# Optimization experiments

Hardware: AMD Instinct MI355X
Metric: run time of the kernel (lower is better)

Reference implementation:

```python
import jax, jax.numpy as jnp
import numpy as np

C, V, L, P, E, HM, H, M, B, T = 512, 32000, 2, 2, 8, 1024, 8, 256, 2, 1024
TOPK, RATIO = 2, 0.5


def setup_inputs() -> dict:
    key = jax.random.key(0)
    ks = iter(jax.random.split(key, 64))

    def nrm(shape, s=0.02):
        return (jax.random.normal(next(ks), shape) * s).astype(jnp.float32)

    return {
        "ids": jax.random.randint(next(ks), (B, T), 0, V, dtype=jnp.int32),
        "embed_w": nrm((V, C)),
        "mem": nrm((M, C)),
        "mp_w": nrm((2 * C, C)), "mp_b": jnp.zeros((C,), jnp.float32),
        "qkv_w": nrm((L, P, C, 3 * C)), "qkv_b": jnp.zeros((L, P, 3 * C), jnp.float32),
        "aw_w": nrm((L, P, C, H)), "aw_b": jnp.zeros((L, P, H), jnp.float32),
        "dscale": jnp.ones((L, P), jnp.float32),
        "mg_w": nrm((L, P * C, C)), "mg_b": jnp.zeros((L, C), jnp.float32),
        "ln_g": jnp.ones((L, C), jnp.float32), "ln_b": jnp.zeros((L, C), jnp.float32),
        "gw": nrm((L, C, E)), "gb": jnp.zeros((L, E), jnp.float32),
        "ew1": nrm((L, E, C, HM)), "eb1": jnp.zeros((L, E, HM), jnp.float32),
        "ew2": nrm((L, E, HM, C)), "eb2": jnp.zeros((L, E, C), jnp.float32),
        "q1w": nrm((L, C, 4 * C)), "q1b": jnp.zeros((L, 4 * C), jnp.float32),
        "q2w": nrm((L, 4 * C, 1)), "q2b": jnp.zeros((L, 1), jnp.float32),
        "errw": nrm((L, C, C)), "errb": jnp.zeros((L, C), jnp.float32),
        "ag1w": nrm((2 * C, 4 * C)), "ag1b": jnp.zeros((4 * C,), jnp.float32),
        "ag2w": nrm((4 * C, C)), "ag2b": jnp.zeros((C,), jnp.float32),
        "pscale": jnp.ones((C,), jnp.float32),
        "head_w": nrm((C, V)), "head_b": jnp.zeros((V,), jnp.float32),
    }


def _forward(ids, embed_w, mem, mp_w, mp_b, qkv_w, qkv_b, aw_w, aw_b, dscale,
             mg_w, mg_b, ln_g, ln_b, gw, gb, ew1, eb1, ew2, eb2,
             q1w, q1b, q2w, q2b, errw, errb, ag1w, ag1b, ag2w, ag2b,
             pscale, head_w, head_b):
    b, t = ids.shape
    hd = C // H
    x = embed_w[ids]                                        # [B,T,C] embedding gather
    # DynamicMemoryBank: attention over memory slots, concat retrieved
    en = jnp.einsum('btc,mc->btm', x, mem)
    ret = jnp.einsum('btm,mc->btc', jax.nn.softmax(en, -1), mem)
    x = jnp.concatenate([x, ret], -1) @ mp_w + mp_b         # memory_proj
    for l in range(L):
        x_in = x
        # IterativeReasoningBlock: stacked MetaCognitiveAttention phases
        h = x_in
        prior = None
        outs = []
        for p in range(P):
            qkv = (h @ qkv_w[l, p] + qkv_b[l, p]).reshape(b, t, 3, H, hd)
            q, k, v = (jnp.moveaxis(qkv[:, :, i], 1, 2) for i in range(3))  # [B,H,T,hd]
            aware = (h.mean(1) @ aw_w[l, p] + aw_b[l, p])[:, :, None, None]  # [B,H,1,1]
            attn = jax.nn.softmax(
                jnp.einsum('bhtd,bhsd->bhts', q, k) * (dscale[l, p] * aware), -1)
            if prior is not None:
                attn = attn + 0.3 * prior
            prior = jax.lax.stop_gradient(attn)
            o = jnp.einsum('bhts,bhsd->bthd', attn, v).reshape(b, t, C)
            h = jax.nn.silu(o)
            outs.append(h)
        merged = jnp.concatenate(outs, -1) @ mg_w[l] + mg_b[l]
        z = merged + x_in
        mu = z.mean(-1, keepdims=True)
        xn = (z - mu) / jnp.sqrt(z.var(-1, keepdims=True) + 1e-5) * ln_g[l] + ln_b[l]
        # MoE: softmax gate, top-k routing, combine (dense-equivalent math)
        scores = jax.nn.softmax(xn @ gw[l] + gb[l], -1)     # [B,T,E]
        vals, idx = jax.lax.top_k(scores, TOPK)
        w = jnp.sum(jax.nn.one_hot(idx, E, dtype=xn.dtype) * vals[..., None], axis=-2)
        eh = jnp.einsum('btc,ech->bteh', xn, ew1[l]) + eb1[l]
        eh = eh * jax.nn.silu(eh)                           # swiglu act: x*silu(x)
        ey = jnp.einsum('bteh,ehc->btec', eh, ew2[l]) + eb2[l]
        moe_out = jnp.einsum('btec,bte->btc', ey, w)
        reason = xn + moe_out * RATIO
        # IntrospectionLayer (quality estimator sees detached x)
        quality = jax.nn.sigmoid(
            jax.nn.silu(jax.lax.stop_gradient(x_in) @ q1w[l] + q1b[l]) @ q2w[l] + q2b[l])
        intro = x_in + 0.3 * ((x_in * (1.0 - quality)) @ errw[l] + errb[l])
        # AutonomousLearningGate
        gate = jnp.tanh(
            jax.nn.silu(jnp.concatenate([reason, intro], -1) @ ag1w + ag1b) @ ag2w + ag2b)
        x = reason + gate * pscale * intro
    return x @ head_w + head_b                              # [B,T,V]


def reference(ids, embed_w, mem, mp_w, mp_b, qkv_w, qkv_b, aw_w, aw_b, dscale,
              mg_w, mg_b, ln_g, ln_b, gw, gb, ew1, eb1, ew2, eb2,
              q1w, q1b, q2w, q2b, errw, errb, ag1w, ag1b, ag2w, ag2b,
              pscale, head_w, head_b):
    return _forward(ids, embed_w, mem, mp_w, mp_b, qkv_w, qkv_b, aw_w, aw_b, dscale,
                    mg_w, mg_b, ln_g, ln_b, gw, gb, ew1, eb1, ew2, eb2,
                    q1w, q1b, q2w, q2b, errw, errb, ag1w, ag1b, ag2w, ag2b,
                    pscale, head_w, head_b)
```

## Files before the change

kernel.cpp:

```cpp
#include <hip/hip_runtime.h>


#define NTOK 2048
#define CDIM 512
#define TLEN 1024
#define NB 2
#define NH 8
#define VDIM 32000

typedef __attribute__((ext_vector_type(4))) float f32x4;
typedef __attribute__((ext_vector_type(8))) __bf16 bf16x8;
typedef __attribute__((ext_vector_type(4))) __bf16 bf16x4;

#define AS1 __attribute__((address_space(1)))
#define AS3 __attribute__((address_space(3)))

__device__ __forceinline__ void g2lds16(const void* g, void* l) {
    __builtin_amdgcn_global_load_lds((const AS1 void*)g, (AS3 void*)l, 16, 0, 0);
}

__global__ __launch_bounds__(256) void gemm_bf16(
    const __bf16* __restrict__ A, int lda,
    const __bf16* __restrict__ B,
    float* __restrict__ C_, int ldc,
    __bf16* __restrict__ Cb, int ldcb,
    const float* __restrict__ bias,
    const float* __restrict__ res, int ldres, float alpha,
    int K, int act)
{
    __shared__ __align__(16) char smem[16384];
    __bf16* As = (__bf16*)smem;
    __bf16* Bs = (__bf16*)(smem + 8192);
    float* cs = (float*)smem;
    const int tid = threadIdx.x;
    const int w = tid >> 6, lane = tid & 63;
    const int nwg = gridDim.x;
    const int q = nwg >> 3, r = nwg & 7;
    const int xcd = blockIdx.x & 7, ii = blockIdx.x >> 3;
    const int swz = (xcd < r) ? xcd * (q + 1) + ii : r * (q + 1) + (xcd - r) * q + ii;
    const int m0 = (swz & 15) * 128, n0 = (swz >> 4) * 128;
    const int wr = (w >> 1) * 64, wc = (w & 1) * 64;
    f32x4 acc[4][4] = {};
    const int mrow = lane & 15, kq = (lane >> 4) * 8;
    for (int k0 = 0; k0 < K; k0 += 32) {
#pragma unroll
        for (int i = 0; i < 2; ++i) {
            const int boff = w * 2048 + i * 1024 + lane * 16;
            const int row = boff >> 6;
            const int ke = (boff & 63) >> 1;
            g2lds16(A + (long)(m0 + row) * lda + k0 + ke, (char*)As + (boff - lane * 16));
            g2lds16(B + (long)(n0 + row) * K + k0 + ke, (char*)Bs + (boff - lane * 16));
        }
        __syncthreads();
        bf16x8 af[4], bfr[4];
#pragma unroll
        for (int i = 0; i < 4; ++i)
            af[i] = *(const bf16x8*)(As + (wr + i * 16 + mrow) * 32 + kq);
#pragma unroll
        for (int j = 0; j < 4; ++j)
            bfr[j] = *(const bf16x8*)(Bs + (wc + j * 16 + mrow) * 32 + kq);
#pragma unroll
        for (int i = 0; i < 4; ++i)
#pragma unroll
            for (int j = 0; j < 4; ++j)
                acc[i][j] = __builtin_amdgcn_mfma_f32_16x16x32_bf16(af[i], bfr[j], acc[i][j], 0, 0, 0);
        __syncthreads();
    }
    const int col_l = lane & 15, row_l = (lane >> 4) * 4;
#pragma unroll
    for (int p = 0; p < 4; ++p) {
        if ((w >> 1) == (p >> 1)) {
#pragma unroll
            for (int iq = 0; iq < 2; ++iq) {
                const int i = (p & 1) * 2 + iq;
#pragma unroll
                for (int j = 0; j < 4; ++j) {
                    const int n_l = wc + j * 16 + col_l;
                    const float bv = bias ? bias[n0 + n_l] : 0.f;
#pragma unroll
                    for (int r2 = 0; r2 < 4; ++r2) {
                        const int lr = iq * 16 + row_l + r2;
// ... 27 lines not shown
            }
        }
        __syncthreads();
    }
}

__global__ __launch_bounds__(256) void gemm64_bf16(
    const __bf16* __restrict__ A, int lda,
    const __bf16* __restrict__ B,
    float* __restrict__ C_, int ldc,
    __bf16* __restrict__ Cb, int ldcb,
    const float* __restrict__ bias,
    const float* __restrict__ res, int ldres, float alpha,
    int K, int act)
{
    __shared__ __align__(16) char smem[8192];
    __bf16* As = (__bf16*)smem;
    __bf16* Bs = (__bf16*)(smem + 4096);
    float* cs = (float*)smem;
    const int tid = threadIdx.x;
    const int w = tid >> 6, lane = tid & 63;
    const int nwg = gridDim.x;
    const int q = nwg >> 3, r = nwg & 7;
    const int xcd = blockIdx.x & 7, ii = blockIdx.x >> 3;
    const int swz = (xcd < r) ? xcd * (q + 1) + ii : r * (q + 1) + (xcd - r) * q + ii;
    const int m0 = (swz & 31) * 64, n0 = (swz >> 5) * 64;
    const int wr = (w >> 1) * 32, wc = (w & 1) * 32;
    f32x4 acc[2][2] = {};
    const int mrow = lane & 15, kq = (lane >> 4) * 8;
    const int arow = tid >> 2, ke = (tid & 3) * 8;
    for (int k0 = 0; k0 < K; k0 += 32) {
        g2lds16(A + (long)(m0 + arow) * lda + k0 + ke, (char*)As + tid * 16 - lane * 16);
        g2lds16(B + (long)(n0 + arow) * K + k0 + ke, (char*)Bs + tid * 16 - lane * 16);
        __syncthreads();
        bf16x8 af[2], bfr[2];
#pragma unroll
        for (int i = 0; i < 2; ++i)
            af[i] = *(const bf16x8*)(As + (wr + i * 16 + mrow) * 32 + kq);
#pragma unroll
        for (int j = 0; j < 2; ++j)
            bfr[j] = *(const bf16x8*)(Bs + (wc + j * 16 + mrow) * 32 + kq);
#pragma unroll
        for (int i = 0; i < 2; ++i)
#pragma unroll
            for (int j = 0; j < 2; ++j)
                acc[i][j] = __builtin_amdgcn_mfma_f32_16x16x32_bf16(af[i], bfr[j], acc[i][j], 0, 0, 0);
        __syncthreads();
    }
    const int col_l = lane & 15, row_l = (lane >> 4) * 4;
#pragma unroll
    for (int p = 0; p < 2; ++p) {
        if ((w >> 1) == p) {
#pragma unroll
            for (int i = 0; i < 2; ++i)
#pragma unroll
                for (int j = 0; j < 2; ++j) {
                    const int n_l = wc + j * 16 + col_l;
                    const float bv = bias ? bias[n0 + n_l] : 0.f;
#pragma unroll
                    for (int r2 = 0; r2 < 4; ++r2) {
                        const int lr = i * 16 + row_l + r2;
                        float v = acc[i][j][r2] + bv;
// ... 65 lines not shown

__global__ __launch_bounds__(256) void moe_g1_k(
    const __bf16* __restrict__ A,
    const __bf16* __restrict__ Bw,
    const float* __restrict__ eb1l,
    const int* __restrict__ offi,
    const int* __restrict__ list,
    __bf16* __restrict__ EHB)
{
    const int m0 = blockIdx.y * 128;
    if (m0 >= offi[8]) return;
    int e = 0;
    while (e < 7 && offi[e + 1] <= m0) ++e;
    const __bf16* B = Bw + (long)e * (1024 * 512);
    const float* bias = eb1l + e * 1024;
    __shared__ __bf16 As[128 * 32];
    __shared__ __bf16 Bs[128 * 32];
    __shared__ int toks[128];
    const int tid = threadIdx.x;
    if (tid < 128) toks[tid] = list[m0 + tid] >> 1;
    __syncthreads();
    const int w = tid >> 6, lane = tid & 63;
    const int n0 = blockIdx.x * 128;
    const int wr = (w >> 1) * 64, wc = (w & 1) * 64;
    f32x4 acc[4][4] = {};
    const int mrow = lane & 15, kq = (lane >> 4) * 8;
    for (int k0 = 0; k0 < 512; k0 += 32) {
#pragma unroll
        for (int i = 0; i < 2; ++i) {
            const int boff = w * 2048 + i * 1024 + lane * 16;
            const int row = boff >> 6;
            const int ke = (boff & 63) >> 1;
            g2lds16(A + (long)toks[row] * 512 + k0 + ke, (char*)As + (boff - lane * 16));
            g2lds16(B + (long)(n0 + row) * 512 + k0 + ke, (char*)Bs + (boff - lane * 16));
        }
        __syncthreads();
        bf16x8 af[4], bfr[4];
#pragma unroll
        for (int i = 0; i < 4; ++i)
            af[i] = *(const bf16x8*)(As + (wr + i * 16 + mrow) * 32 + kq);
#pragma unroll
        for (int j = 0; j < 4; ++j)
            bfr[j] = *(const bf16x8*)(Bs + (wc + j * 16 + mrow) * 32 + kq);
#pragma unroll
        for (int i = 0; i < 4; ++i)
#pragma unroll
            for (int j = 0; j < 4; ++j)
                acc[i][j] = __builtin_amdgcn_mfma_f32_16x16x32_bf16(af[i], bfr[j], acc[i][j], 0, 0, 0);
        __syncthreads();
    }
    const int col_l = lane & 15, row_l = (lane >> 4) * 4;
#pragma unroll
    for (int i = 0; i < 4; ++i)
#pragma unroll
        for (int j = 0; j < 4; ++j) {
            const int n = n0 + wc + j * 16 + col_l;
            const float bv = bias[n];
#pragma unroll
            for (int r = 0; r < 4; ++r) {
                const int g = m0 + wr + i * 16 + row_l + r;
                const float v = acc[i][j][r] + bv;
                EHB[(long)g * 1024 + n] = (__bf16)(v * v / (1.f + __expf(-v)));
            }
        }
}

__global__ __launch_bounds__(256) void moe_g2_k(
    const __bf16* __restrict__ A,
    const __bf16* __restrict__ Bw,
    const float* __restrict__ eb2l,
    const int* __restrict__ offi,
    float* __restrict__ EYS)
{
    const int m0 = blockIdx.y * 128;
    if (m0 >= offi[8]) return;
    int e = 0;
    while (e < 7 && offi[e + 1] <= m0) ++e;
    const __bf16* B = Bw + (long)e * (512 * 1024);
    const float* bias = eb2l + e * 512;
    __shared__ __bf16 As[128 * 32];
    __shared__ __bf16 Bs[128 * 32];
    const int tid = threadIdx.x;
    const int w = tid >> 6, lane = tid & 63;
    const int n0 = blockIdx.x * 128;
    const int wr = (w >> 1) * 64, wc = (w & 1) * 64;
    f32x4 acc[4][4] = {};
    const int mrow = lane & 15, kq = (lane >> 4) * 8;
    for (int k0 = 0; k0 < 1024; k0 += 32) {
#pragma unroll
        for (int i = 0; i < 2; ++i) {
            const int boff = w * 2048 + i * 1024 + lane * 16;
            const int row = boff >> 6;
            const int ke = (boff & 63) >> 1;
            g2lds16(A + (long)(m0 + row) * 1024 + k0 + ke, (char*)As + (boff - lane * 16));
            g2lds16(B + (long)(n0 + row) * 1024 + k0 + ke, (char*)Bs + (boff - lane * 16));
        }
        __syncthreads();
        bf16x8 af[4], bfr[4];
#pragma unroll
        for (int i = 0; i < 4; ++i)
            af[i] = *(const bf16x8*)(As + (wr + i * 16 + mrow) * 32 + kq);
#pragma unroll
        for (int j = 0; j < 4; ++j)
            bfr[j] = *(const bf16x8*)(Bs + (wc + j * 16 + mrow) * 32 + kq);
#pragma unroll
        for (int i = 0; i < 4; ++i)
#pragma unroll
            for (int j = 0; j < 4; ++j)
                acc[i][j] = __builtin_amdgcn_mfma_f32_16x16x32_bf16(af[i], bfr[j], acc[i][j], 0, 0, 0);
        __syncthreads();
    }
    const int col_l = lane & 15, row_l = (lane >> 4) * 4;
#pragma unroll
    for (int i = 0; i < 4; ++i)
#pragma unroll
        for (int j = 0; j < 4; ++j) {
            const int n = n0 + wc + j * 16 + col_l;
            const float bv = bias[n];
#pragma unroll
            for (int r = 0; r < 4; ++r) {
                const int g = m0 + wr + i * 16 + row_l + r;
                EYS[(long)g * 512 + n] = acc[i][j][r] + bv;
            }
        }
}

__global__ __launch_bounds__(256) void reason2_k(const float* __restrict__ xn,
                                                 const float* __restrict__ EYS,
                                                 const float* __restrict__ wv,
                                                 const int* __restrict__ posmap,
                                                 float* __restrict__ reason)
{
    const long i = (long)blockIdx.x * 256 + threadIdx.x;
    const long n = i >> 9;
    const int c = (int)(i & 511);
    const int g0 = posmap[n * 2], g1 = posmap[n * 2 + 1];
    const float v = wv[n * 2] * EYS[(long)g0 * 512 + c] + wv[n * 2 + 1] * EYS[(long)g1 * 512 + c];
// ... 69 lines not shown
    for (int o = 128; o; o >>= 1) { if (t < o) rs[t] += rs[t + o]; __syncthreads(); }
    ob[(long)n * 256 + t] = (__bf16)(e / rs[0]);
}

__global__ __launch_bounds__(256) void concat_bf_k(const float* __restrict__ a,
                                                   const float* __restrict__ b,
                                                   __bf16* __restrict__ o)
{
    const long i = (long)blockIdx.x * 256 + threadIdx.x;
    const long n = i >> 9;
    const int c = (int)(i & 511);
    o[n * 1024 + c]       = (__bf16)a[i];
    o[n * 1024 + 512 + c] = (__bf16)b[i];
}

__global__ __launch_bounds__(64) void meanp_k(const float* __restrict__ A, int lda,
                                              float* __restrict__ part)
{
    const int bid = blockIdx.x;
    const int ts = bid & 15;
    const int cg = (bid >> 4) & 7;
    const int b  = bid >> 7;
    const int c  = cg * 64 + threadIdx.x;
    const float* p = A + ((long)b * TLEN + ts * 64) * lda + c;
    float s = 0.f;
    for (int t = 0; t < 64; ++t) s += p[(long)t * lda];
    part[(long)ts * 1024 + b * 512 + c] = s;
}
__global__ __launch_bounds__(256) void meanr_k(const float* __restrict__ part,
                                               float* __restrict__ hm)
{
    const int i = blockIdx.x * 256 + threadIdx.x;
    float s = 0.f;
    for (int ts = 0; ts < 16; ++ts) s += part[ts * 1024 + i];
    hm[i] = s * (1.f / 1024.f);
}

__global__ __launch_bounds__(64) void aware_k(const float* __restrict__ hm,
                                              const float* __restrict__ aw_w,
                                              const float* __restrict__ aw_b,
                                              int lp, float* __restrict__ out)
{
    const int t = threadIdx.x;
    if (t < NB * NH) {
        const int b = t >> 3, hh = t & 7;
        const float* W = aw_w + (long)lp * CDIM * NH;
        const float* x = hm + b * CDIM;
        float s = aw_b[lp * NH + hh];
        for (int c = 0; c < CDIM; ++c) s += x[c] * W[c * NH + hh];
        out[t] = s;
    }
}

__global__ __launch_bounds__(256) void qkvprep_k(
    const float* __restrict__ qkv,
    const float* __restrict__ dscale, int lp,
    const float* __restrict__ aware,
    __bf16* __restrict__ QKB, __bf16* __restrict__ KB, __bf16* __restrict__ VTB)
{
    const int bh = blockIdx.x >> 4;
    const int tc = blockIdx.x & 15;
    const int b = bh >> 3, h = bh & 7;
    const int tid = threadIdx.x;
    const float sc = dscale[lp] * aware[bh];
    __shared__ float vt[64][68];
    const int row = tid >> 2, c0 = (tid & 3) * 16;
    const long rbase = ((long)(b * 1024 + tc * 64 + row)) * 1536 + h * 64 + c0;
    {
        bf16x8 qo[2], ko[2];
#pragma unroll
        for (int i = 0; i < 2; ++i)
#pragma unroll
            for (int jj = 0; jj < 2; ++jj) {
                const float4 qq = *(const float4*)(qkv + rbase + (i * 2 + jj) * 4);
                const float4 kk = *(const float4*)(qkv + rbase + 512 + (i * 2 + jj) * 4);
                qo[i][jj * 4 + 0] = (__bf16)(qq.x * sc);
                qo[i][jj * 4 + 1] = (__bf16)(qq.y * sc);
                qo[i][jj * 4 + 2] = (__bf16)(qq.z * sc);
                qo[i][jj * 4 + 3] = (__bf16)(qq.w * sc);
                ko[i][jj * 4 + 0] = (__bf16)kk.x;
                ko[i][jj * 4 + 1] = (__bf16)kk.y;
                ko[i][jj * 4 + 2] = (__bf16)kk.z;
                ko[i][jj * 4 + 3] = (__bf16)kk.w;
            }
        const long obase = (long)bh * 65536 + (long)(tc * 64 + row) * 64 + c0;
        *(bf16x8*)(QKB + obase) = qo[0];
        *(bf16x8*)(QKB + obase + 8) = qo[1];
        *(bf16x8*)(KB + obase) = ko[0];
        *(bf16x8*)(KB + obase + 8) = ko[1];
    }
    {
        const long vbase = ((long)(b * 1024 + tc * 64 + row)) * 1536 + 1024 + h * 64 + c0;
#pragma unroll
        for (int i = 0; i < 4; ++i) {
            const float4 v = *(const float4*)(qkv + vbase + i * 4);
            vt[row][c0 + i * 4 + 0] = v.x;
            vt[row][c0 + i * 4 + 1] = v.y;
            vt[row][c0 + i * 4 + 2] = v.z;
            vt[row][c0 + i * 4 + 3] = v.w;
        }
    }
    __syncthreads();
    {
        const int d = row;
        const int s0 = c0;
        bf16x8 o0, o1;
#pragma unroll
        for (int j = 0; j < 8; ++j) o0[j] = (__bf16)vt[s0 + j][d];
#pragma unroll
        for (int j = 0; j < 8; ++j) o1[j] = (__bf16)vt[s0 + 8 + j][d];
        __bf16* dst = VTB + (long)bh * 65536 + (long)d * 1024 + tc * 64 + s0;
        *(bf16x8*)dst = o0;
        *(bf16x8*)(dst + 8) = o1;
    }
}

#define RB 32
__global__ __launch_bounds__(256) void attn2_k(
    const __bf16* __restrict__ QKB,
    const __bf16* __restrict__ KB,
    const __bf16* __restrict__ VTB,
    __bf16* __restrict__ prior,
    int use_prior,
    float* __restrict__ outs, __bf16* __restrict__ outsb, int out_off)
{
    __shared__ __align__(16) __bf16 qs[RB * 64];
    __shared__ __align__(16) __bf16 kv[2][128 * 64];
    __shared__ __align__(16) __bf16 ss[RB * 1024];
    const int tid = threadIdx.x;
    const int w = tid >> 6, lane = tid & 63;
    const int rb = blockIdx.x & 31;
    const int bh = blockIdx.x >> 5;
    const int b = bh >> 3, h = bh & 7;
    const int t0 = rb * RB;
    const long qkbase = (long)bh * 65536;
    const int mrow = lane & 15, kq = (lane >> 4) * 8;

    {
        const int row = tid >> 3, gl = tid & 7;
        const int gs = gl ^ (row & 7);
        g2lds16(QKB + qkbase + (long)(t0 + row) * 64 + gs * 8,
                (char*)qs + tid * 16 - lane * 16);
    }
    {
        for (int it = 0; it < 4; ++it) {
            const int idx = it * 256 + tid;
            const int row = idx >> 3, gl = idx & 7;
            const int gs = gl ^ (row & 7);
            g2lds16(KB + qkbase + (long)row * 64 + gs * 8,
                    (char*)kv[0] + idx * 16 - lane * 16);
        }
        __syncthreads();
        int buf = 0;
        const int ntb = w * 2;
        for (int c = 0; c < 8; ++c) {
            if (c < 7) {
                const int s0n = (c + 1) * 128;
                for (int it = 0; it < 4; ++it) {
                    const int idx = it * 256 + tid;
                    const int row = idx >> 3, gl = idx & 7;
                    const int gs = gl ^ (row & 7);
                    g2lds16(KB + qkbase + (long)(s0n + row) * 64 + gs * 8,
                            (char*)kv[buf ^ 1] + idx * 16 - lane * 16);
                }
            }
            f32x4 accs[2][2] = {};
#pragma unroll
            for (int k0 = 0; k0 < 64; k0 += 32) {
                bf16x8 aq[2], bk[2];
#pragma unroll
                for (int mt = 0; mt < 2; ++mt) {
                    const int r = mt * 16 + mrow;
                    const int col = k0 + kq;
                    aq[mt] = *(const bf16x8*)(qs + r * 64 + (((col >> 3) ^ (r & 7)) << 3));
                }
#pragma unroll
                for (int j = 0; j < 2; ++j) {
                    const int nl = (ntb + j) * 16 + mrow;
                    const int col = k0 + kq;
                    bk[j] = *(const bf16x8*)(kv[buf] + nl * 64 + (((col >> 3) ^ (nl & 7)) << 3));
                }
#pragma unroll
                for (int mt = 0; mt < 2; ++mt)
#pragma unroll
                    for (int j = 0; j < 2; ++j)
                        accs[mt][j] = __builtin_amdgcn_mfma_f32_16x16x32_bf16(aq[mt], bk[j], accs[mt][j], 0, 0, 0);
            }
            const int col_l = lane & 15, row_l = (lane >> 4) * 4;
#pragma unroll
            for (int mt = 0; mt < 2; ++mt)
#pragma unroll
                for (int j = 0; j < 2; ++j) {
                    const int ccol = c * 128 + (ntb + j) * 16 + col_l;
#pragma unroll
                    for (int r = 0; r < 4; ++r) {
                        const int rr = mt * 16 + row_l + r;
                        ss[rr * 1024 + (((ccol >> 3) ^ (rr & 7)) << 3) + (ccol & 7)] = (__bf16)accs[mt][j][r];
                    }
                }
            __syncthreads();
            buf ^= 1;
        }
    }
    for (int it = 0; it < 4; ++it) {
        const int idx = it * 256 + tid;
        const int d = idx >> 4, gl = idx & 15;
        const int gs = gl ^ (d & 7);
        g2lds16(VTB + (long)bh * 65536 + (long)d * 1024 + gs * 8,
                (char*)kv[0] + idx * 16 - lane * 16);
    }
    {
        const int r = tid >> 3;
        const int li = tid & 7;
        const int rsw = r & 7;
        float mx = -1e30f;
        for (int j = 0; j < 16; ++j) {
            const int c = j * 64 + li * 8;
            bf16x8 v = *(const bf16x8*)(ss + r * 1024 + (((c >> 3) ^ rsw) << 3));
#pragma unroll
            for (int q = 0; q < 8; ++q) mx = fmaxf(mx, (float)v[q]);
        }
        mx = fmaxf(mx, __shfl_xor(mx, 1));
        mx = fmaxf(mx, __shfl_xor(mx, 2));
        mx = fmaxf(mx, __shfl_xor(mx, 4));
        float sum = 0.f;
        for (int j = 0; j < 16; ++j) {
            const int c = j * 64 + li * 8;
            __bf16* p = ss + r * 1024 + (((c >> 3) ^ rsw) << 3);
            bf16x8 v = *(const bf16x8*)p;
            bf16x8 e;
#pragma unroll
            for (int q = 0; q < 8; ++q) {
                const float ev = __expf((float)v[q] - mx);
                sum += ev;
                e[q] = (__bf16)ev;
            }
            *(bf16x8*)p = e;
        }
        sum += __shfl_xor(sum, 1);
        sum += __shfl_xor(sum, 2);
        sum += __shfl_xor(sum, 4);
        const float rinv = 1.f / sum;
        const long pbase = ((long)bh * 1024 + t0 + r) * 1024;
        for (int j = 0; j < 16; ++j) {
            const int c = j * 64 + li * 8;
            __bf16* p = ss + r * 1024 + (((c >> 3) ^ rsw) << 3);
            bf16x8 v = *(const bf16x8*)p;
            bf16x8 o;
            if (use_prior) {
                bf16x8 pr = *(const bf16x8*)(prior + pbase + c);
#pragma unroll
                for (int q = 0; q < 8; ++q)
                    o[q] = (__bf16)((float)v[q] * rinv + 0.3f * (float)pr[q]);
            } else {
#pragma unroll
                for (int q = 0; q < 8; ++q)
                    o[q] = (__bf16)((float)v[q] * rinv);
            }
            *(bf16x8*)p = o;
            *(bf16x8*)(prior + pbase + c) = o;
        }
    }
    __syncthreads();
    {
        f32x4 po[2] = {};
        int buf = 0;
        const int mt = w >> 1;
        const int ntb2 = (w & 1) * 2;
        for (int c = 0; c < 8; ++c) {
            if (c < 7) {
                const int s0n = (c + 1) * 128;
                for (int it = 0; it < 4; ++it) {
                    const int idx = it * 256 + tid;
                    const int d = idx >> 4, gl = idx & 15;
                    const int gs = gl ^ (d & 7);
                    g2lds16(VTB + (long)bh * 65536 + (long)d * 1024 + s0n + gs * 8,
                            (char*)kv[buf ^ 1] + idx * 16 - lane * 16);
                }
            }
#pragma unroll
            for (int ks = 0; ks < 4; ++ks) {
                const int r = mt * 16 + mrow;
                const int cola = c * 128 + ks * 32 + kq;
                bf16x8 pa = *(const bf16x8*)(ss + r * 1024 + (((cola >> 3) ^ (r & 7)) << 3));
                bf16x8 vb[2];
#pragma unroll
                for (int j = 0; j < 2; ++j) {
                    const int d = (ntb2 + j) * 16 + mrow;
                    const int colv = ks * 32 + kq;
                    vb[j] = *(const bf16x8*)(kv[buf] + d * 128 + (((colv >> 3) ^ (d & 7)) << 3));
                }
                po[0] = __builtin_amdgcn_mfma_f32_16x16x32_bf16(pa, vb[0], po[0], 0, 0, 0);
                po[1] = __builtin_amdgcn_mfma_f32_16x16x32_bf16(pa, vb[1], po[1], 0, 0, 0);
            }
            __syncthreads();
            buf ^= 1;
        }
        const int col_l = lane & 15, row_l = (lane >> 4) * 4;
#pragma unroll
        for (int j = 0; j < 2; ++j) {
            const int d = out_off + h * 64 + (ntb2 + j) * 16 + col_l;
#pragma unroll
            for (int r = 0; r < 4; ++r) {
                const int trow = t0 + mt * 16 + row_l + r;
                float v = po[j][r];
                v = v / (1.f + __expf(-v));
                const long oi = ((long)(b * 1024 + trow)) * 1024 + d;
                outs[oi] = v;
                outsb[oi] = (__bf16)v;
            }
        }
    }
}

__global__ __launch_bounds__(256) void ln_k(const float* __restrict__ z,
                                            const float* __restrict__ g,
                                            const float* __restrict__ bb,
                                            float* __restrict__ xn,
                                            __bf16* __restrict__ xnb)
{
    const int n = blockIdx.x, t = threadIdx.x;
    __shared__ float rs[256], rq[256];
    const float v0 = z[(long)n * 512 + t];
    const float v1 = z[(long)n * 512 + 256 + t];
// ... 121 lines not shown
    const float* errb    = (const float*)d_in[25];
    const float* ag1w    = (const float*)d_in[26];
    const float* ag1b    = (const float*)d_in[27];
    const float* ag2w    = (const float*)d_in[28];
    const float* ag2b    = (const float*)d_in[29];
    const float* pscale  = (const float*)d_in[30];
    const float* head_w  = (const float*)d_in[31];
    const float* head_b  = (const float*)d_in[32];
    float* out = (float*)d_out;
    float* ws  = (float*)d_ws;

    const long NC = (long)NTOK * CDIM;
    float* X0   = ws;
    float* X1   = ws + NC;
    float* RET  = ws + 2 * NC;
    float* QKV  = ws + 5 * NC;
    float* OUTS = ws + 8 * NC;
    float* EN   = ws + 10 * NC;
    float* SM   = ws + 10 * NC + NC / 2;
    float* PART = SM;
    float* HMEAN= SM + 16384;
    float* AWARE= SM + 17408;
    float* QUAL = SM + 17472;
    float* WV   = SM + 19520;
    int*   EIDX = (int*)(SM + 23616);
    int*   OFFI = (int*)(SM + 27712);
    int*   LIST = (int*)(SM + 27728);
    int*   POSMAP = (int*)(SM + 32848);
    float* R      = ws + 11 * NC;
    __bf16* PRIORB = (__bf16*)R;
    float* Z      = R;
    float* XN     = R + NC;
    float* REASON = R + 2 * NC;
    float* INTRO  = R + 3 * NC;
    float* GATEB  = R + 5 * NC;
    __bf16* EHB   = (__bf16*)(R + 6 * NC);
// ... 53 lines not shown

    embed_k<<<NTOK, 256, 0, stream>>>(ids, embed_w, X0, X0B);
    gemm(X0B, 512, WB_memn, EN, 256, nullptr, 0, nullptr, nullptr, 0, 1.f, 256, 512, 0);
    smrows_k<<<NTOK, 256, 0, stream>>>(EN, ENB);
    gemm(ENB, 256, WB_memt, RET, 512, nullptr, 0, nullptr, nullptr, 0, 1.f, 512, 256, 0);
    concat_bf_k<<<4096, 256, 0, stream>>>(X0, RET, XCATB);
    gemm(XCATB, 1024, WB_mp, X0, 512, X0B, 512, mp_b, nullptr, 0, 1.f, 512, 1024, 0);

    float* xcur = X0;
    float* xalt = X1;
    __bf16* xcurB = X0B;
    __bf16* xaltB = X1B;
    for (int l = 0; l < 2; ++l) {
        for (int p = 0; p < 2; ++p) {
            const int lp = l * 2 + p;
            const float* hptr = (p == 0) ? xcur : OUTS;
            const __bf16* hptrB = (p == 0) ? xcurB : OUTSB;
            const int hlda = (p == 0) ? 512 : 1024;
            gemm(hptrB, hlda, WB_qkv + (long)lp * 1536 * 512, QKV, 1536, nullptr, 0,
                 qkv_b + (long)lp * 1536, nullptr, 0, 1.f, 1536, 512, 0);
            meanp_k<<<256, 64, 0, stream>>>(hptr, hlda, PART);
            meanr_k<<<4, 256, 0, stream>>>(PART, HMEAN);
            aware_k<<<1, 64, 0, stream>>>(HMEAN, aw_w, aw_b, lp, AWARE);
            qkvprep_k<<<256, 256, 0, stream>>>(QKV, dscale, lp, AWARE, QKB, KB, VTB);
            attn2_k<<<512, 256, 0, stream>>>(QKB, KB, VTB, PRIORB,
                                             (p == 1) ? 1 : 0, OUTS, OUTSB, p * CDIM);
        }
        gemm(OUTSB, 1024, WB_mg + (long)l * 512 * 1024, Z, 512, nullptr, 0,
             mg_b + (long)l * 512, xcur, 512, 1.f, 512, 1024, 0);
        ln_k<<<NTOK, 256, 0, stream>>>(Z, ln_g + (long)l * 512, ln_b + (long)l * 512, XN, XNB);
        gate_k<<<NTOK, 64, 0, stream>>>(XN, gw, gb, l, WV, EIDX);
        route_k<<<1, 256, 0, stream>>>(EIDX, OFFI, LIST, POSMAP);
        moe_g1_k<<<dim3(8, 40), 256, 0, stream>>>(XNB, WB_e1 + (long)l * 8 * 524288,
                eb1 + (long)l * 8192, OFFI, LIST, EHB);
        moe_g2_k<<<dim3(4, 40), 256, 0, stream>>>(EHB, WB_e2 + (long)l * 8 * 524288,
                eb2 + (long)l * 4096, OFFI, EYS);
        reason2_k<<<4096, 256, 0, stream>>>(XN, EYS, WV, POSMAP, REASON);
        gemm(xcurB, 512, WB_q1 + (long)l * 2048 * 512, nullptr, 0, Q1BB, 2048,
             q1b + (long)l * 2048, nullptr, 0, 1.f, 2048, 512, 1);
        qual_k<<<NTOK, 256, 0, stream>>>(Q1BB, q2w, q2b, l, QUAL);
        xq_k<<<4096, 256, 0, stream>>>(xcur, QUAL, XQB);
// ... 12 lines not shown
```

Before: 1.597 ms.

## Double-buffer GEMM and attention LDS loads, emit bf16 QKV, fuse mean/aware kernels

All MFMA GEMM kernels (generic, 64-tile, MoE up and down) and the attention K/V staging now double-buffer LDS, prefetching the next k-tile with global_load_lds and using explicit vmcnt waits and raw barriers. The aim is to hide global-load latency behind MFMA work. Separately, the QKV projection writes bf16 instead of fp32, and qkvprep reads bf16 directly, which halves that traffic. The per-head mean is computed from the bf16 activations, and the mean-reduce and aware kernels are merged into one launch. Attention no longer writes an fp32 copy of its output. The costs are twice the LDS per block, which can lower occupancy, and slight precision changes from computing the mean on bf16 inputs.

```diff
diff --git a/kernel.cpp b/kernel.cpp
--- a/kernel.cpp
+++ b/kernel.cpp
@@ -18,6 +18,12 @@
 __device__ __forceinline__ void g2lds16(const void* g, void* l) {
     __builtin_amdgcn_global_load_lds((const AS1 void*)g, (AS3 void*)l, 16, 0, 0);
 }
+
+#define SBAR() __builtin_amdgcn_s_barrier()
+#define SCHED0() __builtin_amdgcn_sched_barrier(0)
+#define WAITV4() asm volatile("s_waitcnt vmcnt(4)" ::: "memory")
+#define WAITV2() asm volatile("s_waitcnt vmcnt(2)" ::: "memory")
+#define WAITV0() asm volatile("s_waitcnt vmcnt(0)" ::: "memory")
 
 __global__ __launch_bounds__(256) void gemm_bf16(
     const __bf16* __restrict__ A, int lda,
@@ -28,9 +34,7 @@
     const float* __restrict__ res, int ldres, float alpha,
     int K, int act)
 {
-    __shared__ __align__(16) char smem[16384];
-    __bf16* As = (__bf16*)smem;
-    __bf16* Bs = (__bf16*)(smem + 8192);
+    __shared__ __align__(16) char smem[32768];
     float* cs = (float*)smem;
     const int tid = threadIdx.x;
     const int w = tid >> 6, lane = tid & 63;
@@ -42,16 +46,32 @@
     const int wr = (w >> 1) * 64, wc = (w & 1) * 64;
     f32x4 acc[4][4] = {};
     const int mrow = lane & 15, kq = (lane >> 4) * 8;
-    for (int k0 = 0; k0 < K; k0 += 32) {
+
+    auto STAGE = [&](int s, int k0) {
 #pragma unroll
         for (int i = 0; i < 2; ++i) {
             const int boff = w * 2048 + i * 1024 + lane * 16;
             const int row = boff >> 6;
             const int ke = (boff & 63) >> 1;
-            g2lds16(A + (long)(m0 + row) * lda + k0 + ke, (char*)As + (boff - lane * 16));
-            g2lds16(B + (long)(n0 + row) * K + k0 + ke, (char*)Bs + (boff - lane * 16));
-        }
-        __syncthreads();
+            g2lds16(A + (long)(m0 + row) * lda + k0 + ke,
+                    smem + s * 16384 + (boff - lane * 16));
+            g2lds16(B + (long)(n0 + row) * K + k0 + ke,
+                    smem + s * 16384 + 8192 + (boff - lane * 16));
+        }
+    };
+    const int nt = K >> 5;
+    STAGE(0, 0);
+    for (int t = 0; t < nt; ++t) {
+        const int cur = t & 1;
+        if (t + 1 < nt) {
+            STAGE(cur ^ 1, (t + 1) << 5);
+            SCHED0(); WAITV4();
+        } else {
+            SCHED0(); WAITV0();
+        }
+        SBAR(); SCHED0();
+        const __bf16* As = (const __bf16*)(smem + cur * 16384);
+        const __bf16* Bs = (const __bf16*)(smem + cur * 16384 + 8192);
         bf16x8 af[4], bfr[4];
 #pragma unroll
         for (int i = 0; i < 4; ++i)
@@ -64,7 +84,7 @@
 #pragma unroll
             for (int j = 0; j < 4; ++j)
                 acc[i][j] = __builtin_amdgcn_mfma_f32_16x16x32_bf16(af[i], bfr[j], acc[i][j], 0, 0, 0);
-        __syncthreads();
+        SCHED0(); SBAR();
     }
     const int col_l = lane & 15, row_l = (lane >> 4) * 4;
 #pragma unroll
@@ -122,9 +142,7 @@
     const float* __restrict__ res, int ldres, float alpha,
     int K, int act)
 {
-    __shared__ __align__(16) char smem[8192];
-    __bf16* As = (__bf16*)smem;
-    __bf16* Bs = (__bf16*)(smem + 4096);
+    __shared__ __align__(16) char smem[16384];
     float* cs = (float*)smem;
     const int tid = threadIdx.x;
     const int w = tid >> 6, lane = tid & 63;
@@ -137,10 +155,26 @@
     f32x4 acc[2][2] = {};
     const int mrow = lane & 15, kq = (lane >> 4) * 8;
     const int arow = tid >> 2, ke = (tid & 3) * 8;
-    for (int k0 = 0; k0 < K; k0 += 32) {
-        g2lds16(A + (long)(m0 + arow) * lda + k0 + ke, (char*)As + tid * 16 - lane * 16);
-        g2lds16(B + (long)(n0 + arow) * K + k0 + ke, (char*)Bs + tid * 16 - lane * 16);
-        __syncthreads();
+
+    auto STAGE = [&](int s, int k0) {
+        g2lds16(A + (long)(m0 + arow) * lda + k0 + ke,
+                smem + s * 8192 + (tid * 16 - lane * 16));
+        g2lds16(B + (long)(n0 + arow) * K + k0 + ke,
+                smem + s * 8192 + 4096 + (tid * 16 - lane * 16));
+    };
+    const int nt = K >> 5;
+    STAGE(0, 0);
+    for (int t = 0; t < nt; ++t) {
+        const int cur = t & 1;
+        if (t + 1 < nt) {
+            STAGE(cur ^ 1, (t + 1) << 5);
+            SCHED0(); WAITV2();
+        } else {
+            SCHED0(); WAITV0();
+        }
+        SBAR(); SCHED0();
+        const __bf16* As = (const __bf16*)(smem + cur * 8192);
+        const __bf16* Bs = (const __bf16*)(smem + cur * 8192 + 4096);
         bf16x8 af[2], bfr[2];
 #pragma unroll
         for (int i = 0; i < 2; ++i)
@@ -153,7 +187,7 @@
 #pragma unroll
             for (int j = 0; j < 2; ++j)
                 acc[i][j] = __builtin_amdgcn_mfma_f32_16x16x32_bf16(af[i], bfr[j], acc[i][j], 0, 0, 0);
-        __syncthreads();
+        SCHED0(); SBAR();
     }
     const int col_l = lane & 15, row_l = (lane >> 4) * 4;
 #pragma unroll
@@ -249,8 +283,7 @@
     while (e < 7 && offi[e + 1] <= m0) ++e;
     const __bf16* B = Bw + (long)e * (1024 * 512);
     const float* bias = eb1l + e * 1024;
-    __shared__ __bf16 As[128 * 32];
-    __shared__ __bf16 Bs[128 * 32];
+    __shared__ __align__(16) char smem[32768];
     __shared__ int toks[128];
     const int tid = threadIdx.x;
     if (tid < 128) toks[tid] = list[m0 + tid] >> 1;
@@ -260,16 +293,35 @@
     const int wr = (w >> 1) * 64, wc = (w & 1) * 64;
     f32x4 acc[4][4] = {};
     const int mrow = lane & 15, kq = (lane >> 4) * 8;
-    for (int k0 = 0; k0 < 512; k0 += 32) {
+    int tk[2], boffs[2], kes[2], brow[2];
+#pragma unroll
+    for (int i = 0; i < 2; ++i) {
+        boffs[i] = w * 2048 + i * 1024 + lane * 16;
+        brow[i] = boffs[i] >> 6;
+        kes[i] = (boffs[i] & 63) >> 1;
+        tk[i] = toks[brow[i]];
+    }
+    auto STAGE = [&](int s, int k0) {
 #pragma unroll
         for (int i = 0; i < 2; ++i) {
-            const int boff = w * 2048 + i * 1024 + lane * 16;
-            const int row = boff >> 6;
-            const int ke = (boff & 63) >> 1;
-            g2lds16(A + (long)toks[row] * 512 + k0 + ke, (char*)As + (boff - lane * 16));
-            g2lds16(B + (long)(n0 + row) * 512 + k0 + ke, (char*)Bs + (boff - lane * 16));
-        }
-        __syncthreads();
+            g2lds16(A + (long)tk[i] * 512 + k0 + kes[i],
+                    smem + s * 16384 + (boffs[i] - lane * 16));
+            g2lds16(B + (long)(n0 + brow[i]) * 512 + k0 + kes[i],
+                    smem + s * 16384 + 8192 + (boffs[i] - lane * 16));
+        }
+    };
+    STAGE(0, 0);
+    for (int t = 0; t < 16; ++t) {
+        const int cur = t & 1;
+        if (t + 1 < 16) {
+            STAGE(cur ^ 1, (t + 1) << 5);
+            SCHED0(); WAITV4();
+        } else {
+            SCHED0(); WAITV0();
+        }
+        SBAR(); SCHED0();
+        const __bf16* As = (const __bf16*)(smem + cur * 16384);
+        const __bf16* Bs = (const __bf16*)(smem + cur * 16384 + 8192);
         bf16x8 af[4], bfr[4];
 #pragma unroll
         for (int i = 0; i < 4; ++i)
@@ -282,7 +334,7 @@
 #pragma unroll
             for (int j = 0; j < 4; ++j)
                 acc[i][j] = __builtin_amdgcn_mfma_f32_16x16x32_bf16(af[i], bfr[j], acc[i][j], 0, 0, 0);
-        __syncthreads();
+        SCHED0(); SBAR();
     }
     const int col_l = lane & 15, row_l = (lane >> 4) * 4;
 #pragma unroll
@@ -292,9 +344,9 @@
             const int n = n0 + wc + j * 16 + col_l;
             const float bv = bias[n];
 #pragma unroll
-            for (int r = 0; r < 4; ++r) {
-                const int g = m0 + wr + i * 16 + row_l + r;
-                const float v = acc[i][j][r] + bv;
+            for (int r2 = 0; r2 < 4; ++r2) {
+                const int g = m0 + wr + i * 16 + row_l + r2;
+                const float v = acc[i][j][r2] + bv;
                 EHB[(long)g * 1024 + n] = (__bf16)(v * v / (1.f + __expf(-v)));
             }
         }
@@ -313,24 +365,37 @@
     while (e < 7 && offi[e + 1] <= m0) ++e;
     const __bf16* B = Bw + (long)e * (512 * 1024);
     const float* bias = eb2l + e * 512;
-    __shared__ __bf16 As[128 * 32];
-    __shared__ __bf16 Bs[128 * 32];
+    __shared__ __align__(16) char smem[32768];
     const int tid = threadIdx.x;
     const int w = tid >> 6, lane = tid & 63;
     const int n0 = blockIdx.x * 128;
     const int wr = (w >> 1) * 64, wc = (w & 1) * 64;
     f32x4 acc[4][4] = {};
     const int mrow = lane & 15, kq = (lane >> 4) * 8;
-    for (int k0 = 0; k0 < 1024; k0 += 32) {
+    auto STAGE = [&](int s, int k0) {
 #pragma unroll
         for (int i = 0; i < 2; ++i) {
             const int boff = w * 2048 + i * 1024 + lane * 16;
             const int row = boff >> 6;
             const int ke = (boff & 63) >> 1;
-            g2lds16(A + (long)(m0 + row) * 1024 + k0 + ke, (char*)As + (boff - lane * 16));
-            g2lds16(B + (long)(n0 + row) * 1024 + k0 + ke, (char*)Bs + (boff - lane * 16));
-        }
-        __syncthreads();
+            g2lds16(A + (long)(m0 + row) * 1024 + k0 + ke,
+                    smem + s * 16384 + (boff - lane * 16));
+            g2lds16(B + (long)(n0 + row) * 1024 + k0 + ke,
+                    smem + s * 16384 + 8192 + (boff - lane * 16));
+        }
+    };
+    STAGE(0, 0);
+    for (int t = 0; t < 32; ++t) {
+        const int cur = t & 1;
+        if (t + 1 < 32) {
+            STAGE(cur ^ 1, (t + 1) << 5);
+            SCHED0(); WAITV4();
+        } else {
+            SCHED0(); WAITV0();
+        }
+        SBAR(); SCHED0();
+        const __bf16* As = (const __bf16*)(smem + cur * 16384);
+        const __bf16* Bs = (const __bf16*)(smem + cur * 16384 + 8192);
         bf16x8 af[4], bfr[4];
 #pragma unroll
         for (int i = 0; i < 4; ++i)
@@ -343,7 +408,7 @@
 #pragma unroll
             for (int j = 0; j < 4; ++j)
                 acc[i][j] = __builtin_amdgcn_mfma_f32_16x16x32_bf16(af[i], bfr[j], acc[i][j], 0, 0, 0);
-        __syncthreads();
+        SCHED0(); SBAR();
     }
     const int col_l = lane & 15, row_l = (lane >> 4) * 4;
 #pragma unroll
@@ -353,9 +418,9 @@
             const int n = n0 + wc + j * 16 + col_l;
             const float bv = bias[n];
 #pragma unroll
-            for (int r = 0; r < 4; ++r) {
-                const int g = m0 + wr + i * 16 + row_l + r;
-                EYS[(long)g * 512 + n] = acc[i][j][r] + bv;
+            for (int r2 = 0; r2 < 4; ++r2) {
+                const int g = m0 + wr + i * 16 + row_l + r2;
+                EYS[(long)g * 512 + n] = acc[i][j][r2] + bv;
             }
         }
 }
@@ -455,46 +520,45 @@
     o[n * 1024 + 512 + c] = (__bf16)b[i];
 }
 
-__global__ __launch_bounds__(64) void meanp_k(const float* __restrict__ A, int lda,
-                                              float* __restrict__ part)
+__global__ __launch_bounds__(64) void meanpb_k(const __bf16* __restrict__ A, int lda,
+                                               float* __restrict__ part)
 {
     const int bid = blockIdx.x;
     const int ts = bid & 15;
     const int cg = (bid >> 4) & 7;
     const int b  = bid >> 7;
     const int c  = cg * 64 + threadIdx.x;
-    const float* p = A + ((long)b * TLEN + ts * 64) * lda + c;
+    const __bf16* p = A + ((long)b * TLEN + ts * 64) * lda + c;
     float s = 0.f;
-    for (int t = 0; t < 64; ++t) s += p[(long)t * lda];
+    for (int t = 0; t < 64; ++t) s += (float)p[(long)t * lda];
     part[(long)ts * 1024 + b * 512 + c] = s;
 }
-__global__ __launch_bounds__(256) void meanr_k(const float* __restrict__ part,
-                                               float* __restrict__ hm)
-{
-    const int i = blockIdx.x * 256 + threadIdx.x;
+
+__global__ __launch_bounds__(256) void mraware_k(const float* __restrict__ part,
+                                                 const float* __restrict__ aw_w,
+                                                 const float* __restrict__ aw_b,
+                                                 int lp, float* __restrict__ aware)
+{
+    __shared__ float hm[1024];
+    const int t = threadIdx.x;
+    for (int i = t; i < 1024; i += 256) {
+        float s = 0.f;
+        for (int ts = 0; ts < 16; ++ts) s += part[ts * 1024 + i];
+        hm[i] = s * (1.f / 1024.f);
+    }
+    __syncthreads();
+    const int g = t >> 4, li = t & 15;
+    const int b = g >> 3, hh = g & 7;
+    const float* W = aw_w + (long)lp * CDIM * NH;
     float s = 0.f;
-    for (int ts = 0; ts < 16; ++ts) s += part[ts * 1024 + i];
-    hm[i] = s * (1.f / 1024.f);
-}
-
-__global__ __launch_bounds__(64) void aware_k(const float* __restrict__ hm,
-                                              const float* __restrict__ aw_w,
-                                              const float* __restrict__ aw_b,
-                                              int lp, float* __restrict__ out)
-{
-    const int t = threadIdx.x;
-    if (t < NB * NH) {
-        const int b = t >> 3, hh = t & 7;
-        const float* W = aw_w + (long)lp * CDIM * NH;
-        const float* x = hm + b * CDIM;
-        float s = aw_b[lp * NH + hh];
-        for (int c = 0; c < CDIM; ++c) s += x[c] * W[c * NH + hh];
-        out[t] = s;
-    }
+    for (int c = li; c < CDIM; c += 16) s += hm[b * CDIM + c] * W[c * NH + hh];
+    s += __shfl_xor(s, 1); s += __shfl_xor(s, 2);
+    s += __shfl_xor(s, 4); s += __shfl_xor(s, 8);
+    if (li == 0) aware[g] = s + aw_b[lp * NH + hh];
 }
 
 __global__ __launch_bounds__(256) void qkvprep_k(
-    const float* __restrict__ qkv,
+    const __bf16* __restrict__ qkvb,
     const float* __restrict__ dscale, int lp,
     const float* __restrict__ aware,
     __bf16* __restrict__ QKB, __bf16* __restrict__ KB, __bf16* __restrict__ VTB)
@@ -504,52 +568,34 @@
     const int b = bh >> 3, h = bh & 7;
     const int tid = threadIdx.x;
     const float sc = dscale[lp] * aware[bh];
-    __shared__ float vt[64][68];
+    __shared__ __bf16 vt[64][72];
     const int row = tid >> 2, c0 = (tid & 3) * 16;
     const long rbase = ((long)(b * 1024 + tc * 64 + row)) * 1536 + h * 64 + c0;
+    const long obase = (long)bh * 65536 + (long)(tc * 64 + row) * 64 + c0;
     {
-        bf16x8 qo[2], ko[2];
-#pragma unroll
-        for (int i = 0; i < 2; ++i)
-#pragma unroll
-            for (int jj = 0; jj < 2; ++jj) {
-                const float4 qq = *(const float4*)(qkv + rbase + (i * 2 + jj) * 4);
-                const float4 kk = *(const float4*)(qkv + rbase + 512 + (i * 2 + jj) * 4);
-                qo[i][jj * 4 + 0] = (__bf16)(qq.x * sc);
-                qo[i][jj * 4 + 1] = (__bf16)(qq.y * sc);
-                qo[i][jj * 4 + 2] = (__bf16)(qq.z * sc);
-                qo[i][jj * 4 + 3] = (__bf16)(qq.w * sc);
-                ko[i][jj * 4 + 0] = (__bf16)kk.x;
-                ko[i][jj * 4 + 1] = (__bf16)kk.y;
-                ko[i][jj * 4 + 2] = (__bf16)kk.z;
-                ko[i][jj * 4 + 3] = (__bf16)kk.w;
-            }
-        const long obase = (long)bh * 65536 + (long)(tc * 64 + row) * 64 + c0;
-        *(bf16x8*)(QKB + obase) = qo[0];
-        *(bf16x8*)(QKB + obase + 8) = qo[1];
-        *(bf16x8*)(KB + obase) = ko[0];
-        *(bf16x8*)(KB + obase + 8) = ko[1];
-    }
+        const bf16x8 q0 = *(const bf16x8*)(qkvb + rbase);
+        const bf16x8 q1 = *(const bf16x8*)(qkvb + rbase + 8);
+        bf16x8 o0, o1;
+#pragma unroll
+        for (int j = 0; j < 8; ++j) {
+            o0[j] = (__bf16)((float)q0[j] * sc);
+            o1[j] = (__bf16)((float)q1[j] * sc);
+        }
+        *(bf16x8*)(QKB + obase) = o0;
+        *(bf16x8*)(QKB + obase + 8) = o1;
+        *(bf16x8*)(KB + obase)     = *(const bf16x8*)(qkvb + rbase + 512);
+        *(bf16x8*)(KB + obase + 8) = *(const bf16x8*)(qkvb + rbase + 520);
+        *(bf16x8*)(&vt[row][c0])     = *(const bf16x8*)(qkvb + rbase + 1024);
+        *(bf16x8*)(&vt[row][c0 + 8]) = *(const bf16x8*)(qkvb + rbase + 1032);
+    }
+    __syncthreads();
     {
-        const long vbase = ((long)(b * 1024 + tc * 64 + row)) * 1536 + 1024 + h * 64 + c0;
-#pragma unroll
-        for (int i = 0; i < 4; ++i) {
-            const float4 v = *(const float4*)(qkv + vbase + i * 4);
-            vt[row][c0 + i * 4 + 0] = v.x;
-            vt[row][c0 + i * 4 + 1] = v.y;
-            vt[row][c0 + i * 4 + 2] = v.z;
-            vt[row][c0 + i * 4 + 3] = v.w;
-        }
-    }
-    __syncthreads();
-    {
-        const int d = row;
-        const int s0 = c0;
+        const int d = row, s0 = c0;
         bf16x8 o0, o1;
 #pragma unroll
-        for (int j = 0; j < 8; ++j) o0[j] = (__bf16)vt[s0 + j][d];
-#pragma unroll
-        for (int j = 0; j < 8; ++j) o1[j] = (__bf16)vt[s0 + 8 + j][d];
+        for (int j = 0; j < 8; ++j) o0[j] = vt[s0 + j][d];
+#pragma unroll
+        for (int j = 0; j < 8; ++j) o1[j] = vt[s0 + 8 + j][d];
         __bf16* dst = VTB + (long)bh * 65536 + (long)d * 1024 + tc * 64 + s0;
         *(bf16x8*)dst = o0;
         *(bf16x8*)(dst + 8) = o1;
@@ -563,7 +609,7 @@
     const __bf16* __restrict__ VTB,
     __bf16* __restrict__ prior,
     int use_prior,
-    float* __restrict__ outs, __bf16* __restrict__ outsb, int out_off)
+    __bf16* __restrict__ outsb, int out_off)
 {
     __shared__ __align__(16) __bf16 qs[RB * 64];
     __shared__ __align__(16) __bf16 kv[2][128 * 64];
@@ -583,37 +629,47 @@
         g2lds16(QKB + qkbase + (long)(t0 + row) * 64 + gs * 8,
                 (char*)qs + tid * 16 - lane * 16);
     }
-    {
+    auto stageK = [&](int s0n, int bufi) {
+#pragma unroll
         for (int it = 0; it < 4; ++it) {
             const int idx = it * 256 + tid;
             const int row = idx >> 3, gl = idx & 7;
             const int gs = gl ^ (row & 7);
-            g2lds16(KB + qkbase + (long)row * 64 + gs * 8,
-                    (char*)kv[0] + idx * 16 - lane * 16);
-        }
-        __syncthreads();
+            g2lds16(KB + qkbase + (long)(s0n + row) * 64 + gs * 8,
+                    (char*)kv[bufi] + idx * 16 - lane * 16);
+        }
+    };
+    auto stageV = [&](int s0n, int bufi) {
+#pragma unroll
+        for (int it = 0; it < 4; ++it) {
+            const int idx = it * 256 + tid;
+            const int d = idx >> 4, gl = idx & 15;
+            const int gs = gl ^ (d & 7);
+            g2lds16(VTB + (long)bh * 65536 + (long)d * 1024 + s0n + gs * 8,
+                    (char*)kv[bufi] + idx * 16 - lane * 16);
+        }
+    };
+    {
+        stageK(0, 0);
         int buf = 0;
         const int ntb = w * 2;
         for (int c = 0; c < 8; ++c) {
             if (c < 7) {
-                const int s0n = (c + 1) * 128;
-                for (int it = 0; it < 4; ++it) {
-                    const int idx = it * 256 + tid;
-                    const int row = idx >> 3, gl = idx & 7;
-                    const int gs = gl ^ (row & 7);
-                    g2lds16(KB + qkbase + (long)(s0n + row) * 64 + gs * 8,
-                            (char*)kv[buf ^ 1] + idx * 16 - lane * 16);
-                }
-            }
+                stageK((c + 1) * 128, buf ^ 1);
+                SCHED0(); WAITV4();
+            } else {
+                SCHED0(); WAITV0();
+            }
+            SBAR(); SCHED0();
             f32x4 accs[2][2] = {};
 #pragma unroll
             for (int k0 = 0; k0 < 64; k0 += 32) {
                 bf16x8 aq[2], bk[2];
 #pragma unroll
                 for (int mt = 0; mt < 2; ++mt) {
-                    const int r = mt * 16 + mrow;
+                    const int rr = mt * 16 + mrow;
                     const int col = k0 + kq;
-                    aq[mt] = *(const bf16x8*)(qs + r * 64 + (((col >> 3) ^ (r & 7)) << 3));
+                    aq[mt] = *(const bf16x8*)(qs + rr * 64 + (((col >> 3) ^ (rr & 7)) << 3));
                 }
 #pragma unroll
                 for (int j = 0; j < 2; ++j) {
@@ -634,32 +690,27 @@
                 for (int j = 0; j < 2; ++j) {
                     const int ccol = c * 128 + (ntb + j) * 16 + col_l;
 #pragma unroll
-                    for (int r = 0; r < 4; ++r) {
-                        const int rr = mt * 16 + row_l + r;
-                        ss[rr * 1024 + (((ccol >> 3) ^ (rr & 7)) << 3) + (ccol & 7)] = (__bf16)accs[mt][j][r];
+                    for (int r2 = 0; r2 < 4; ++r2) {
+                        const int rr = mt * 16 + row_l + r2;
+                        ss[rr * 1024 + (((ccol >> 3) ^ (rr & 7)) << 3) + (ccol & 7)] = (__bf16)accs[mt][j][r2];
                     }
                 }
-            __syncthreads();
+            SCHED0(); SBAR();
             buf ^= 1;
         }
     }
-    for (int it = 0; it < 4; ++it) {
-        const int idx = it * 256 + tid;
-        const int d = idx >> 4, gl = idx & 15;
-        const int gs = gl ^ (d & 7);
-        g2lds16(VTB + (long)bh * 65536 + (long)d * 1024 + gs * 8,
-                (char*)kv[0] + idx * 16 - lane * 16);
-    }
+    __syncthreads();
+    stageV(0, 0);
     {
-        const int r = tid >> 3;
+        const int r2 = tid >> 3;
         const int li = tid & 7;
-        const int rsw = r & 7;
+        const int rsw = r2 & 7;
         float mx = -1e30f;
         for (int j = 0; j < 16; ++j) {
             const int c = j * 64 + li * 8;
-            bf16x8 v = *(const bf16x8*)(ss + r * 1024 + (((c >> 3) ^ rsw) << 3));
-#pragma unroll
-            for (int q = 0; q < 8; ++q) mx = fmaxf(mx, (float)v[q]);
+            bf16x8 v = *(const bf16x8*)(ss + r2 * 1024 + (((c >> 3) ^ rsw) << 3));
+#pragma unroll
+            for (int q2 = 0; q2 < 8; ++q2) mx = fmaxf(mx, (float)v[q2]);
         }
         mx = fmaxf(mx, __shfl_xor(mx, 1));
         mx = fmaxf(mx, __shfl_xor(mx, 2));
@@ -667,42 +718,43 @@
         float sum = 0.f;
         for (int j = 0; j < 16; ++j) {
             const int c = j * 64 + li * 8;
-            __bf16* p = ss + r * 1024 + (((c >> 3) ^ rsw) << 3);
+            __bf16* p = ss + r2 * 1024 + (((c >> 3) ^ rsw) << 3);
             bf16x8 v = *(const bf16x8*)p;
-            bf16x8 e;
-#pragma unroll
-            for (int q = 0; q < 8; ++q) {
-                const float ev = __expf((float)v[q] - mx);
+            bf16x8 ee;
+#pragma unroll
+            for (int q2 = 0; q2 < 8; ++q2) {
+                const float ev = __expf((float)v[q2] - mx);
                 sum += ev;
-                e[q] = (__bf16)ev;
-            }
-            *(bf16x8*)p = e;
+                ee[q2] = (__bf16)ev;
+            }
+            *(bf16x8*)p = ee;
         }
         sum += __shfl_xor(sum, 1);
         sum += __shfl_xor(sum, 2);
         sum += __shfl_xor(sum, 4);
         const float rinv = 1.f / sum;
-        const long pbase = ((long)bh * 1024 + t0 + r) * 1024;
+        const long pbase = ((long)bh * 1024 + t0 + r2) * 1024;
         for (int j = 0; j < 16; ++j) {
             const int c = j * 64 + li * 8;
-            __bf16* p = ss + r * 1024 + (((c >> 3) ^ rsw) << 3);
+            __bf16* p = ss + r2 * 1024 + (((c >> 3) ^ rsw) << 3);
             bf16x8 v = *(const bf16x8*)p;
             bf16x8 o;
             if (use_prior) {
                 bf16x8 pr = *(const bf16x8*)(prior + pbase + c);
 #pragma unroll
-                for (int q = 0; q < 8; ++q)
-                    o[q] = (__bf16)((float)v[q] * rinv + 0.3f * (float)pr[q]);
+                for (int q2 = 0; q2 < 8; ++q2)
+                    o[q2] = (__bf16)((float)v[q2] * rinv + 0.3f * (float)pr[q2]);
             } else {
 #pragma unroll
-                for (int q = 0; q < 8; ++q)
-                    o[q] = (__bf16)((float)v[q] * rinv);
+                for (int q2 = 0; q2 < 8; ++q2)
+                    o[q2] = (__bf16)((float)v[q2] * rinv);
             }
             *(bf16x8*)p = o;
             *(bf16x8*)(prior + pbase + c) = o;
         }
     }
-    __syncthreads();
+    asm volatile("s_waitcnt lgkmcnt(0)" ::: "memory");
+    SCHED0(); SBAR(); SCHED0();
     {
         f32x4 po[2] = {};
         int buf = 0;
@@ -710,20 +762,17 @@
         const int ntb2 = (w & 1) * 2;
         for (int c = 0; c < 8; ++c) {
             if (c < 7) {
-                const int s0n = (c + 1) * 128;
-                for (int it = 0; it < 4; ++it) {
-                    const int idx = it * 256 + tid;
-                    const int d = idx >> 4, gl = idx & 15;
-                    const int gs = gl ^ (d & 7);
-                    g2lds16(VTB + (long)bh * 65536 + (long)d * 1024 + s0n + gs * 8,
-                            (char*)kv[buf ^ 1] + idx * 16 - lane * 16);
-                }
-            }
+                stageV((c + 1) * 128, buf ^ 1);
+                SCHED0(); WAITV4();
+            } else {
+                SCHED0(); WAITV0();
+            }
+            SBAR(); SCHED0();
 #pragma unroll
             for (int ks = 0; ks < 4; ++ks) {
-                const int r = mt * 16 + mrow;
+                const int rr = mt * 16 + mrow;
                 const int cola = c * 128 + ks * 32 + kq;
-                bf16x8 pa = *(const bf16x8*)(ss + r * 1024 + (((cola >> 3) ^ (r & 7)) << 3));
+                bf16x8 pa = *(const bf16x8*)(ss + rr * 1024 + (((cola >> 3) ^ (rr & 7)) << 3));
                 bf16x8 vb[2];
 #pragma unroll
                 for (int j = 0; j < 2; ++j) {
@@ -734,7 +783,7 @@
                 po[0] = __builtin_amdgcn_mfma_f32_16x16x32_bf16(pa, vb[0], po[0], 0, 0, 0);
                 po[1] = __builtin_amdgcn_mfma_f32_16x16x32_bf16(pa, vb[1], po[1], 0, 0, 0);
             }
-            __syncthreads();
+            SCHED0(); SBAR();
             buf ^= 1;
         }
         const int col_l = lane & 15, row_l = (lane >> 4) * 4;
@@ -742,13 +791,11 @@
         for (int j = 0; j < 2; ++j) {
             const int d = out_off + h * 64 + (ntb2 + j) * 16 + col_l;
 #pragma unroll
-            for (int r = 0; r < 4; ++r) {
-                const int trow = t0 + mt * 16 + row_l + r;
-                float v = po[j][r];
+            for (int r2 = 0; r2 < 4; ++r2) {
+                const int trow = t0 + mt * 16 + row_l + r2;
+                float v = po[j][r2];
                 v = v / (1.f + __expf(-v));
-                const long oi = ((long)(b * 1024 + trow)) * 1024 + d;
-                outs[oi] = v;
-                outsb[oi] = (__bf16)v;
+                outsb[((long)(b * 1024 + trow)) * 1024 + d] = (__bf16)v;
             }
         }
     }
@@ -900,12 +947,10 @@
     float* X0   = ws;
     float* X1   = ws + NC;
     float* RET  = ws + 2 * NC;
-    float* QKV  = ws + 5 * NC;
-    float* OUTS = ws + 8 * NC;
+    __bf16* QKVB = (__bf16*)(ws + 5 * NC);
     float* EN   = ws + 10 * NC;
     float* SM   = ws + 10 * NC + NC / 2;
     float* PART = SM;
-    float* HMEAN= SM + 16384;
     float* AWARE= SM + 17408;
     float* QUAL = SM + 17472;
     float* WV   = SM + 19520;
@@ -989,17 +1034,15 @@
     for (int l = 0; l < 2; ++l) {
         for (int p = 0; p < 2; ++p) {
             const int lp = l * 2 + p;
-            const float* hptr = (p == 0) ? xcur : OUTS;
             const __bf16* hptrB = (p == 0) ? xcurB : OUTSB;
             const int hlda = (p == 0) ? 512 : 1024;
-            gemm(hptrB, hlda, WB_qkv + (long)lp * 1536 * 512, QKV, 1536, nullptr, 0,
+            gemm(hptrB, hlda, WB_qkv + (long)lp * 1536 * 512, nullptr, 0, QKVB, 1536,
                  qkv_b + (long)lp * 1536, nullptr, 0, 1.f, 1536, 512, 0);
-            meanp_k<<<256, 64, 0, stream>>>(hptr, hlda, PART);
-            meanr_k<<<4, 256, 0, stream>>>(PART, HMEAN);
-            aware_k<<<1, 64, 0, stream>>>(HMEAN, aw_w, aw_b, lp, AWARE);
-            qkvprep_k<<<256, 256, 0, stream>>>(QKV, dscale, lp, AWARE, QKB, KB, VTB);
+            meanpb_k<<<256, 64, 0, stream>>>(hptrB, hlda, PART);
+            mraware_k<<<1, 256, 0, stream>>>(PART, aw_w, aw_b, lp, AWARE);
+            qkvprep_k<<<256, 256, 0, stream>>>(QKVB, dscale, lp, AWARE, QKB, KB, VTB);
             attn2_k<<<512, 256, 0, stream>>>(QKB, KB, VTB, PRIORB,
-                                             (p == 1) ? 1 : 0, OUTS, OUTSB, p * CDIM);
+                                             (p == 1) ? 1 : 0, OUTSB, p * CDIM);
         }
         gemm(OUTSB, 1024, WB_mg + (long)l * 512 * 1024, Z, 512, nullptr, 0,
              mg_b + (long)l * 512, xcur, 512, 1.f, 512, 1024, 0);
```

Result: slower. 1.777 ms (+11.3%).
